# Optimization experiments

Hardware: AMD Instinct MI355X
Metric: run time of the kernel (lower is better)

The kernel has to match this reference:

```python
import jax, jax.numpy as jnp
import numpy as np

H = 16          # num_heads
EPS = 1e-6      # RMSNorm eps


def setup_inputs() -> dict:
    key = jax.random.key(0)
    ks = jax.random.split(key, 5)
    B, N, D = 4, 4096, 1024
    x = jax.random.normal(ks[0], (B, N, D), dtype=jnp.float32)
    q = jax.random.normal(ks[1], (D,), dtype=jnp.float32)
    k = jax.random.normal(ks[2], (D,), dtype=jnp.float32)
    log_decay = jax.random.normal(ks[3], (H,), dtype=jnp.float32)
    norm_weight = jnp.ones((D,), dtype=jnp.float32)
    o_w = jax.random.normal(ks[4], (D, D), dtype=jnp.float32) * 0.02
    return {"x": x, "q": q, "k": k, "log_decay": log_decay,
            "norm_weight": norm_weight, "o_w": o_w}


def reference(x, q, k, log_decay, norm_weight, o_w):
    b, n, dm = x.shape
    dh = dm // H
    qh = q.reshape(H, dh)            # per-head query vector (constant over b, n)
    kh = k.reshape(H, dh)            # per-head key vector
    v = x.reshape(b, n, H, dh)       # values = input tokens
    # exp(logsigmoid(a)) == sigmoid(a): per-head decay in (0, 1)
    lam = jax.nn.sigmoid(log_decay)  # (H,)

    def step(S, v_t):
        # S: (b, H, dh, dh) recurrent state;  v_t: (b, H, dh)
        S = lam[None, :, None, None] * S + kh[None, :, :, None] * v_t[:, :, None, :]
        o_t = jnp.einsum('hd,bhdv->bhv', qh, S)
        return S, o_t

    S0 = jnp.zeros((b, H, dh, dh), dtype=x.dtype)
    _, o = jax.lax.scan(step, S0, jnp.moveaxis(v, 1, 0))  # o: (n, b, H, dh)
    o = jnp.moveaxis(o, 0, 1).reshape(b, n, dm)

    # RMSNorm over the channel dim
    o = o * jax.lax.rsqrt(jnp.mean(o * o, axis=-1, keepdims=True) + EPS) * norm_weight
    # o_proj (no bias)
    return o @ o_w.T
```

## Files before the change

kernel.cpp:

```cpp
#include <hip/hip_runtime.h>
#include <hip/hip_bf16.h>
#include <cstdint>
#include <cstddef>

#define HH   16
#define BB   4
#define NN   4096
#define DD   1024
#define MM   (BB * NN)
#define NC   256
#define LC   16
#define EPSV 1e-6f

typedef short short8 __attribute__((ext_vector_type(8)));
typedef float floatx4 __attribute__((ext_vector_type(4)));

__device__ __forceinline__ void async_copy16(const void* g, void* l) {
    __builtin_amdgcn_global_load_lds(
        (const __attribute__((address_space(1))) void*)g,
        (__attribute__((address_space(3))) void*)l, 16, 0, 0);
}

__device__ __forceinline__ uint2 pack_bf16x4(float a, float b, float c, float d) {
    union { __hip_bfloat16 h[4]; uint2 u; } cv;
    cv.h[0] = __float2bfloat16(a); cv.h[1] = __float2bfloat16(b);
    cv.h[2] = __float2bfloat16(c); cv.h[3] = __float2bfloat16(d);
    return cv.u;
}

__device__ __forceinline__ float sigmoidf(float a) {
    return 1.f / (1.f + expf(-a));
}

__global__ void k_prep(const float* __restrict__ x, const float* __restrict__ ld,
                       float* __restrict__ E, const float* __restrict__ ow,
                       const float* __restrict__ nw, __hip_bfloat16* __restrict__ wp) {
    int g = blockIdx.x;
    if (g < BB * NC) {
        int b = g >> 8, c = g & (NC - 1);
        int j4 = threadIdx.x;
        float lam = sigmoidf(ld[j4 >> 4]);
        const float4* xp = (const float4*)(x + ((size_t)(b * NN + c * LC)) * DD) + j4;
        float4 e = {0.f, 0.f, 0.f, 0.f};
        #pragma unroll
        for (int t = 0; t < LC; ++t) {
            float4 v = xp[(size_t)t * (DD / 4)];
            e.x = fmaf(lam, e.x, v.x); e.y = fmaf(lam, e.y, v.y);
            e.z = fmaf(lam, e.z, v.z); e.w = fmaf(lam, e.w, v.w);
        }
        ((float4*)(E + (size_t)g * DD))[j4] = e;
    } else {
        size_t i4 = (size_t)(g - BB * NC) * 256 + threadIdx.x;
        int j = (int)((i4 * 4) & (DD - 1));
        float4 v = ((const float4*)ow)[i4];
        ((uint2*)wp)[i4] = pack_bf16x4(v.x * nw[j], v.y * nw[j + 1],
                                       v.z * nw[j + 2], v.w * nw[j + 3]);
    }
}

__global__ void k_carry(const float* __restrict__ ld, float* __restrict__ E) {
    __shared__ float tile[NC][33];
    int b = blockIdx.x >> 5, jg = blockIdx.x & 31;
    int tid = threadIdx.x;
    int cc = tid >> 5, jj = tid & 31;
    #pragma unroll
    for (int it = 0; it < NC / 8; ++it) {
        int c = it * 8 + cc;
        tile[c][jj] = E[(size_t)(b * NC + c) * DD + jg * 32 + jj];
    }
    __syncthreads();
    if (tid < 32) {
        int j = jg * 32 + tid;
        float lam = sigmoidf(ld[j >> 6]);
        float lamL = lam;
        lamL *= lamL; lamL *= lamL; lamL *= lamL; lamL *= lamL;
        float p = 0.f;
        for (int c = 0; c < NC; ++c) {
            float e = tile[c][tid];
            tile[c][tid] = p;
            p = fmaf(lamL, p, e);
        }
    }
    __syncthreads();
    #pragma unroll
    for (int it = 0; it < NC / 8; ++it) {
        int c = it * 8 + cc;
        E[(size_t)(b * NC + c) * DD + jg * 32 + jj] = tile[c][jj];
    }
}

__global__ void k_scan(const float* __restrict__ x, const float* __restrict__ q,
                       const float* __restrict__ k, const float* __restrict__ ld,
                       const float* __restrict__ P, __hip_bfloat16* __restrict__ obf,
                       float* __restrict__ sumsq) {
    __shared__ float ssq[4][LC];
    int b = blockIdx.x >> 8, c = blockIdx.x & (NC - 1);
    int j4 = threadIdx.x;
    int h = j4 >> 4;
    float lam = sigmoidf(ld[h]);
    float4 q4 = ((const float4*)q)[j4];
    float4 k4 = ((const float4*)k)[j4];
    float ch = q4.x * k4.x + q4.y * k4.y + q4.z * k4.z + q4.w * k4.w;
    #pragma unroll
    for (int off = 1; off < 16; off <<= 1) ch += __shfl_xor(ch, off);
    int row0 = b * NN + c * LC;
    int lane = threadIdx.x & 63, w = threadIdx.x >> 6;
    const float4* xp = (const float4*)(x + (size_t)row0 * DD) + j4;
    float4 y = ((const float4*)(P + (size_t)blockIdx.x * DD))[j4];
    #pragma unroll
    for (int t = 0; t < LC; ++t) {
        float4 v = xp[(size_t)t * (DD / 4)];
        y.x = fmaf(lam, y.x, v.x); y.y = fmaf(lam, y.y, v.y);
        y.z = fmaf(lam, y.z, v.z); y.w = fmaf(lam, y.w, v.w);
        float ox = ch * y.x, oy = ch * y.y, oz = ch * y.z, ow = ch * y.w;
        ((uint2*)(obf + (size_t)(row0 + t) * DD))[j4] = pack_bf16x4(ox, oy, oz, ow);
        float s = ox * ox + oy * oy + oz * oz + ow * ow;
        #pragma unroll
        for (int off = 32; off > 0; off >>= 1) s += __shfl_xor(s, off);
        if (lane == 0) ssq[w][t] = s;
    }
    __syncthreads();
    if (threadIdx.x < LC) {
        int t = threadIdx.x;
        sumsq[row0 + t] = ssq[0][t] + ssq[1][t] + ssq[2][t] + ssq[3][t];
    }
}

#define GEMM_STAGE_A(SLOT, S)                                                  \
  do {                                                                         \
    char* _da = (char*)&lds[SLOT][0][0] + w * 1024;                            \
    _Pragma("unroll") for (int _i = 0; _i < 2; ++_i)                           \
      async_copy16(Ag + (size_t)(m0 + _i * 128 + rr) * 1024 + (S) * 32 + oo * 8, \
                   _da + _i * 8192);                                           \
  } while (0)

#define GEMM_STAGE_B(SLOT, S)                                                  \
  do {                                                                         \
    char* _db = (char*)&lds[SLOT][1][0] + w * 1024;                            \
    _Pragma("unroll") for (int _i = 0; _i < 2; ++_i)                           \
      async_copy16(Wg + (size_t)(n0 + _i * 128 + rr) * 1024 + (S) * 32 + oo * 8, \
                   _db + _i * 8192);                                           \
  } while (0)

#define PHASE_A(SLOT, DO_STAGE, S3)                                            \
  do {                                                                         \
    const short* _a = &lds[SLOT][0][0];                                        \
    const short* _b = &lds[SLOT][1][0];                                        \
    _Pragma("unroll") for (int nt = 0; nt < 4; ++nt)                           \
      bf[nt] = *(const short8*)(_b + (brow_base + nt * 16) * 32 + p_rd * 8);   \
    _Pragma("unroll") for (int mt = 0; mt < 4; ++mt)                           \
      af[mt] = *(const short8*)(_a + (arow_base + mt * 16) * 32 + p_rd * 8);   \
    if (DO_STAGE) GEMM_STAGE_A((S3) & 3, S3);                                  \
    __builtin_amdgcn_s_barrier();                                              \
    asm volatile("s_waitcnt lgkmcnt(0)" ::: "memory");                         \
    __builtin_amdgcn_s_setprio(1);                                             \
    _Pragma("unroll") for (int mt = 0; mt < 4; ++mt) {                         \
      _Pragma("unroll") for (int nt = 0; nt < 4; ++nt)                         \
        acc[mt][nt] = __builtin_amdgcn_mfma_f32_16x16x32_bf16(                 \
            af[mt], bf[nt], acc[mt][nt], 0, 0, 0);                             \
    }                                                                          \
    __builtin_amdgcn_s_setprio(0);                                             \
    __builtin_amdgcn_s_barrier();                                              \
  } while (0)

#define PHASE_B(SLOT, DO_STAGE, S3)                                            \
  do {                                                                         \
    const short* _a = &lds[SLOT][0][0];                                        \
    _Pragma("unroll") for (int mt = 0; mt < 4; ++mt)                           \
      af[mt] = *(const short8*)(_a + (arow_base + 64 + mt * 16) * 32 + p_rd * 8); \
    if (DO_STAGE) GEMM_STAGE_B((S3) & 3, S3);                                  \
    __builtin_amdgcn_s_barrier();                                              \
    asm volatile("s_waitcnt lgkmcnt(0)" ::: "memory");                         \
    __builtin_amdgcn_s_setprio(1);                                             \
    _Pragma("unroll") for (int mt = 0; mt < 4; ++mt) {                         \
      _Pragma("unroll") for (int nt = 0; nt < 4; ++nt)                         \
        acc[4 + mt][nt] = __builtin_amdgcn_mfma_f32_16x16x32_bf16(             \
            af[mt], bf[nt], acc[4 + mt][nt], 0, 0, 0);                         \
    }                                                                          \
    __builtin_amdgcn_s_setprio(0);                                             \
  } while (0)

__launch_bounds__(512, 2)
__global__ void k_gemm(const __hip_bfloat16* __restrict__ A,
                       const __hip_bfloat16* __restrict__ W,
                       const float* __restrict__ sumsq, float* __restrict__ out) {
    __shared__ __attribute__((aligned(16))) short lds[4][2][256 * 32];
    const int tid = threadIdx.x;
    const int lane = tid & 63, w = tid >> 6;
    const int wm = w >> 2, wn = w & 3;
    const int g = blockIdx.x;
    const int xcd = g & 7, idx = g >> 3;
    const int bm = xcd * 8 + (idx >> 2);
    const int bn = idx & 3;
    const int m0 = bm * 256, n0 = bn * 256;
    const short* Ag = (const short*)A;
    const short* Wg = (const short*)W;

    const int rr = tid >> 2;
    const int oo = (tid & 3) ^ ((rr >> 1) & 3);

    const int p_rd = (lane >> 4) ^ (((lane & 15) >> 1) & 3);
    const int arow_base = wm * 128 + (lane & 15);
    const int brow_base = wn * 64 + (lane & 15);

    floatx4 acc[8][4] = {};
    short8 af[4], bf[4];

    GEMM_STAGE_A(0, 0); GEMM_STAGE_B(0, 0);
    GEMM_STAGE_A(1, 1); GEMM_STAGE_B(1, 1);
    GEMM_STAGE_A(2, 2); GEMM_STAGE_B(2, 2);
    asm volatile("s_waitcnt vmcnt(8)" ::: "memory");
    __builtin_amdgcn_s_barrier();

    #pragma unroll 1
    for (int s = 0; s < 29; ++s) {
        PHASE_A(s & 3, 1, s + 3);
        PHASE_B(s & 3, 1, s + 3);
        asm volatile("s_waitcnt vmcnt(8)" ::: "memory");
        __builtin_amdgcn_s_barrier();
    }
    PHASE_A(1, 0, 0); PHASE_B(1, 0, 0);
    asm volatile("s_waitcnt vmcnt(4)" ::: "memory");
    __builtin_amdgcn_s_barrier();
    PHASE_A(2, 0, 0); PHASE_B(2, 0, 0);
    asm volatile("s_waitcnt vmcnt(0)" ::: "memory");
    __builtin_amdgcn_s_barrier();
    PHASE_A(3, 0, 0); PHASE_B(3, 0, 0);

    #pragma unroll
    for (int mt = 0; mt < 8; ++mt) {
        #pragma unroll
        for (int r = 0; r < 4; ++r) {
            int mrow = m0 + wm * 128 + mt * 16 + (lane >> 4) * 4 + r;
            float rs = rsqrtf(sumsq[mrow] * (1.f / 1024.f) + EPSV);
            #pragma unroll
            for (int nt = 0; nt < 4; ++nt) {
                int col = n0 + wn * 64 + nt * 16 + (lane & 15);
                out[(size_t)mrow * 1024 + col] = acc[mt][nt][r] * rs;
            }
        }
    }
}

extern "C" void kernel_launch(void* const* d_in, const int* in_sizes, int n_in,
                              void* d_out, int out_size, void* d_ws, size_t ws_size,
                              hipStream_t stream) {
    const float* x  = (const float*)d_in[0];
    const float* q  = (const float*)d_in[1];
    const float* k  = (const float*)d_in[2];
    const float* ld = (const float*)d_in[3];
    const float* nw = (const float*)d_in[4];
    const float* ow = (const float*)d_in[5];
    float* out = (float*)d_out;

    char* ws = (char*)d_ws;
    float* sumsq = (float*)(ws + 256);
    float* E     = (float*)(ws + 65792);
    __hip_bfloat16* Wp  = (__hip_bfloat16*)(ws + 4260096);
    __hip_bfloat16* Obf = (__hip_bfloat16*)(ws + 6357248);

    k_prep<<<BB * NC + (DD * DD / 4) / 256, 256, 0, stream>>>(x, ld, E, ow, nw, Wp);
    k_carry<<<BB * 32, 256, 0, stream>>>(ld, E);
    k_scan<<<BB * NC, 256, 0, stream>>>(x, q, k, ld, E, Obf, sumsq);
    k_gemm<<<(MM / 256) * (DD / 256), 512, 0, stream>>>(Obf, Wp, sumsq, out);
}
```

Measured before the change: 175.3 us.

## Fuse carry propagation into scan by recomputing chunk prefix per block

Removes the separate carry kernel. Each scan block instead recomputes its incoming state by looping over all previous chunk sums with the chunk-level decay. The x loads for the chunk are hoisted into registers before this loop. This saves a launch and a serial kernel, but adds quadratic redundant reads of the chunk-sum buffer and load imbalance across blocks.

```diff
diff --git a/kernel.cpp b/kernel.cpp
--- a/kernel.cpp
+++ b/kernel.cpp
@@ -58,40 +58,10 @@
     }
 }
 
-__global__ void k_carry(const float* __restrict__ ld, float* __restrict__ E) {
-    __shared__ float tile[NC][33];
-    int b = blockIdx.x >> 5, jg = blockIdx.x & 31;
-    int tid = threadIdx.x;
-    int cc = tid >> 5, jj = tid & 31;
-    #pragma unroll
-    for (int it = 0; it < NC / 8; ++it) {
-        int c = it * 8 + cc;
-        tile[c][jj] = E[(size_t)(b * NC + c) * DD + jg * 32 + jj];
-    }
-    __syncthreads();
-    if (tid < 32) {
-        int j = jg * 32 + tid;
-        float lam = sigmoidf(ld[j >> 6]);
-        float lamL = lam;
-        lamL *= lamL; lamL *= lamL; lamL *= lamL; lamL *= lamL;
-        float p = 0.f;
-        for (int c = 0; c < NC; ++c) {
-            float e = tile[c][tid];
-            tile[c][tid] = p;
-            p = fmaf(lamL, p, e);
-        }
-    }
-    __syncthreads();
-    #pragma unroll
-    for (int it = 0; it < NC / 8; ++it) {
-        int c = it * 8 + cc;
-        E[(size_t)(b * NC + c) * DD + jg * 32 + jj] = tile[c][jj];
-    }
-}
-
+__launch_bounds__(256)
 __global__ void k_scan(const float* __restrict__ x, const float* __restrict__ q,
                        const float* __restrict__ k, const float* __restrict__ ld,
-                       const float* __restrict__ P, __hip_bfloat16* __restrict__ obf,
+                       const float* __restrict__ E, __hip_bfloat16* __restrict__ obf,
                        float* __restrict__ sumsq) {
     __shared__ float ssq[4][LC];
     int b = blockIdx.x >> 8, c = blockIdx.x & (NC - 1);
@@ -103,15 +73,30 @@
     float ch = q4.x * k4.x + q4.y * k4.y + q4.z * k4.z + q4.w * k4.w;
     #pragma unroll
     for (int off = 1; off < 16; off <<= 1) ch += __shfl_xor(ch, off);
+
     int row0 = b * NN + c * LC;
     int lane = threadIdx.x & 63, w = threadIdx.x >> 6;
+
     const float4* xp = (const float4*)(x + (size_t)row0 * DD) + j4;
-    float4 y = ((const float4*)(P + (size_t)blockIdx.x * DD))[j4];
+    float4 v[LC];
+    #pragma unroll
+    for (int t = 0; t < LC; ++t) v[t] = xp[(size_t)t * (DD / 4)];
+
+    float lamL = lam;
+    lamL *= lamL; lamL *= lamL; lamL *= lamL; lamL *= lamL;
+    float4 y = {0.f, 0.f, 0.f, 0.f};
+    const float4* Ep = (const float4*)E + (size_t)(b * NC) * (DD / 4) + j4;
+    #pragma unroll 4
+    for (int cp = 0; cp < c; ++cp) {
+        float4 e = Ep[(size_t)cp * (DD / 4)];
+        y.x = fmaf(lamL, y.x, e.x); y.y = fmaf(lamL, y.y, e.y);
+        y.z = fmaf(lamL, y.z, e.z); y.w = fmaf(lamL, y.w, e.w);
+    }
+
     #pragma unroll
     for (int t = 0; t < LC; ++t) {
-        float4 v = xp[(size_t)t * (DD / 4)];
-        y.x = fmaf(lam, y.x, v.x); y.y = fmaf(lam, y.y, v.y);
-        y.z = fmaf(lam, y.z, v.z); y.w = fmaf(lam, y.w, v.w);
+        y.x = fmaf(lam, y.x, v[t].x); y.y = fmaf(lam, y.y, v[t].y);
+        y.z = fmaf(lam, y.z, v[t].z); y.w = fmaf(lam, y.w, v[t].w);
         float ox = ch * y.x, oy = ch * y.y, oz = ch * y.z, ow = ch * y.w;
         ((uint2*)(obf + (size_t)(row0 + t) * DD))[j4] = pack_bf16x4(ox, oy, oz, ow);
         float s = ox * ox + oy * oy + oz * oz + ow * ow;
@@ -260,7 +245,6 @@
     __hip_bfloat16* Obf = (__hip_bfloat16*)(ws + 6357248);
 
     k_prep<<<BB * NC + (DD * DD / 4) / 256, 256, 0, stream>>>(x, ld, E, ow, nw, Wp);
-    k_carry<<<BB * 32, 256, 0, stream>>>(ld, E);
     k_scan<<<BB * NC, 256, 0, stream>>>(x, q, k, ld, E, Obf, sumsq);
     k_gemm<<<(MM / 256) * (DD / 256), 512, 0, stream>>>(Obf, Wp, sumsq, out);
 }
```

After: 198.4 us. 13.2% more time.
